# Kernel tuning notes

Hardware: AMD Instinct MI355X
Metric: run time of the kernel (lower is better)

Reference implementation:

```python
import jax, jax.numpy as jnp
import numpy as np

B, L, S = 8, 8192, 512
DQ, DC = 256, 768
H, DH = 8, 64
INNER = H * DH


def setup_inputs() -> dict:
    key = jax.random.key(0)
    ks = jax.random.split(key, 8)
    std_q = 1.0 / np.sqrt(DQ)
    std_c = 1.0 / np.sqrt(DC)
    std_o = 1.0 / np.sqrt(INNER)
    return {
        "x": jax.random.normal(ks[0], (B, L, DQ), jnp.float32),
        "context": jax.random.normal(ks[1], (B, S, DC), jnp.float32),
        "seq_lens": jax.random.randint(ks[2], (B,), 1, L + 1, jnp.int32),
        "Wq": jax.random.normal(ks[3], (DQ, INNER), jnp.float32) * std_q,
        "Wk": jax.random.normal(ks[4], (DC, INNER), jnp.float32) * std_c,
        "Wv": jax.random.normal(ks[5], (DC, INNER), jnp.float32) * std_c,
        "Wo": jax.random.normal(ks[6], (INNER, DQ), jnp.float32) * std_o,
        "bo": jnp.zeros((DQ,), jnp.float32),
    }


def reference(x, context, seq_lens, Wq, Wk, Wv, Wo, bo):
    # x: [B, L, DQ] padded jagged voxel features; seq_lens: valid count per batch.
    # Equivalent to the per-batch SDPA loop: each batch's queries attend over
    # that batch's full (unmasked) context of S tokens.
    scale = 1.0 / np.sqrt(DH)
    q = (x @ Wq).reshape(B, L, H, DH).transpose(0, 2, 1, 3)        # [B,H,L,DH]
    k = (context @ Wk).reshape(B, S, H, DH).transpose(0, 2, 1, 3)  # [B,H,S,DH]
    v = (context @ Wv).reshape(B, S, H, DH).transpose(0, 2, 1, 3)  # [B,H,S,DH]
    scores = jnp.einsum("bhld,bhsd->bhls", q, k) * scale           # [B,H,L,S]
    attn = jax.nn.softmax(scores, axis=-1)
    out = jnp.einsum("bhls,bhsd->bhld", attn, v)                   # [B,H,L,DH]
    out = out.transpose(0, 2, 1, 3).reshape(B, L, INNER)
    out = out @ Wo + bo                                            # [B,L,DQ]
    valid = (jnp.arange(L)[None, :] < seq_lens[:, None])[..., None]
    return jnp.where(valid, out, 0.0)
```

## Files before the change

kernel.cpp:

```cpp
#include <hip/hip_runtime.h>
#include <hip/hip_bf16.h>

#define DEV __device__ __forceinline__

typedef float f32x4 __attribute__((ext_vector_type(4)));
typedef unsigned short u16x4 __attribute__((ext_vector_type(4)));
typedef unsigned short u16x8 __attribute__((ext_vector_type(8)));
typedef __bf16 bf16x8 __attribute__((ext_vector_type(8)));

DEV unsigned short f2b(float f) { __bf16 h = (__bf16)f; return __builtin_bit_cast(unsigned short, h); }
DEV bf16x8 asbf8(u16x8 v) { return __builtin_bit_cast(bf16x8, v); }

#define MFMA(a, b, c) __builtin_amdgcn_mfma_f32_16x16x32_bf16((a), (b), (c), 0, 0, 0)

constexpr float QSCALE = 0.18033688011112042f;
constexpr float MFIX = 20.0f;

__global__ __launch_bounds__(256) void convert_weights(
    const float* __restrict__ Wq, const float* __restrict__ Wk,
    const float* __restrict__ Wv, const float* __restrict__ Wo,
    unsigned short* __restrict__ WqT, unsigned short* __restrict__ WkvT,
    unsigned short* __restrict__ WoT)
{
  int i = blockIdx.x * 256 + threadIdx.x;
  if (i < 131072) {
    int n = i >> 8, k = i & 255;
    WqT[i] = f2b(Wq[k * 512 + n] * QSCALE);
  } else if (i < 131072 + 786432) {
    int j = i - 131072;
    int n = j / 768, k = j - n * 768;
    float v = (n < 512) ? Wk[k * 512 + n] : Wv[k * 512 + (n - 512)];
    WkvT[j] = f2b(v);
  } else {
    int j = i - 917504;
    int n = j >> 9, k = j & 511;
    WoT[j] = f2b(Wo[k * 256 + n]);
  }
}

template<int KDIM, int NCOLS, bool AF32, int EPI>
DEV void proj_body(int bx, int by, char* smem,
                   const float* __restrict__ Af, const unsigned short* __restrict__ Ab,
                   const unsigned short* __restrict__ BT, const int* __restrict__ seq_lens,
                   unsigned short* __restrict__ out0, unsigned short* __restrict__ out1,
                   float* __restrict__ outf, const float* __restrict__ bo)
{
  constexpr int WC = NCOLS / 4;
  constexpr int NCT = WC / 16;
  constexpr int KSTEPS = KDIM / 32;
  constexpr int ASZ = AF32 ? (64 * 36 * 4) : (64 * 40 * 2);
  const int t = threadIdx.x;
  const int wid = t >> 6, lane = t & 63;
  const int q = lane & 15, g = lane >> 4;
  const int row0 = bx * 64;
  const int wcol = by * NCOLS + wid * WC;

  int sl = 0;
  if (EPI == 0 || EPI == 2) {
    sl = seq_lens[row0 >> 13];
    if ((row0 & 8191) >= sl) {
      if (EPI == 2 && by == 0) {
        f32x4 z = {0.f, 0.f, 0.f, 0.f};
        float* o = outf + (size_t)row0 * 256;
        #pragma unroll
        for (int i = 0; i < 16; ++i)
          *(f32x4*)(o + (size_t)(i * 256 + t) * 4) = z;
      }
      return;
    }
  }

  const int ar0 = t >> 3, akc = (t & 7) * 4;
  const int br0 = t >> 2, bkc = (t & 3) * 8;

  f32x4 acc[4][NCT];
  #pragma unroll
  for (int i = 0; i < 4; ++i)
    #pragma unroll
    for (int j = 0; j < NCT; ++j) acc[i][j] = {0.f, 0.f, 0.f, 0.f};

  f32x4 a0, a1;
  u16x8 ab;
  if (AF32) {
    a0 = *(const f32x4*)(Af + (size_t)(row0 + ar0) * KDIM + akc);
    a1 = *(const f32x4*)(Af + (size_t)(row0 + 32 + ar0) * KDIM + akc);
    float* Lf = (float*)smem;
    *(f32x4*)(Lf + ar0 * 36 + akc) = a0;
    *(f32x4*)(Lf + (32 + ar0) * 36 + akc) = a1;
  } else {
    ab = *(const u16x8*)(Ab + (size_t)(row0 + br0) * KDIM + bkc);
    *(u16x8*)((unsigned short*)smem + br0 * 40 + bkc) = ab;
  }
  bf16x8 bcur[NCT];
  #pragma unroll
  for (int ct = 0; ct < NCT; ++ct)
    bcur[ct] = asbf8(*(const u16x8*)(BT + (size_t)(wcol + ct * 16 + q) * KDIM + g * 8));
  __syncthreads();

  #pragma unroll 2
  for (int st = 0; st < KSTEPS; ++st) {
    const int cur = st & 1;
    const int k1 = (st + 1) * 32;

    if (st + 1 < KSTEPS) {
      if (AF32) {
        a0 = *(const f32x4*)(Af + (size_t)(row0 + ar0) * KDIM + k1 + akc);
        a1 = *(const f32x4*)(Af + (size_t)(row0 + 32 + ar0) * KDIM + k1 + akc);
      } else {
        ab = *(const u16x8*)(Ab + (size_t)(row0 + br0) * KDIM + k1 + bkc);
      }
    }
    bf16x8 bnx[NCT];
    if (st + 1 < KSTEPS) {
      #pragma unroll
      for (int ct = 0; ct < NCT; ++ct)
        bnx[ct] = asbf8(*(const u16x8*)(BT + (size_t)(wcol + ct * 16 + q) * KDIM + k1 + g * 8));
    }

    bf16x8 af[4];
    if (AF32) {
      const float* Lf = (const float*)(smem + cur * ASZ);
      #pragma unroll
      for (int rt = 0; rt < 4; ++rt) {
        const float* pp = Lf + (rt * 16 + q) * 36 + g * 8;
        f32x4 lo = *(const f32x4*)pp;
        f32x4 hi = *(const f32x4*)(pp + 4);
        u16x8 u;
        u[0] = f2b(lo[0]); u[1] = f2b(lo[1]); u[2] = f2b(lo[2]); u[3] = f2b(lo[3]);
        u[4] = f2b(hi[0]); u[5] = f2b(hi[1]); u[6] = f2b(hi[2]); u[7] = f2b(hi[3]);
        af[rt] = asbf8(u);
      }
    } else {
      const unsigned short* Lb = (const unsigned short*)(smem + cur * ASZ);
      #pragma unroll
      for (int rt = 0; rt < 4; ++rt)
        af[rt] = asbf8(*(const u16x8*)(Lb + (rt * 16 + q) * 40 + g * 8));
    }

    #pragma unroll
    for (int ct = 0; ct < NCT; ++ct)
      #pragma unroll
      for (int rt = 0; rt < 4; ++rt)
        acc[rt][ct] = MFMA(af[rt], bcur[ct], acc[rt][ct]);

    if (st + 1 < KSTEPS) {
      if (AF32) {
        float* Lf = (float*)(smem + (cur ^ 1) * ASZ);
        *(f32x4*)(Lf + ar0 * 36 + akc) = a0;
        *(f32x4*)(Lf + (32 + ar0) * 36 + akc) = a1;
      } else {
        *(u16x8*)((unsigned short*)(smem + (cur ^ 1) * ASZ) + br0 * 40 + bkc) = ab;
      }
      #pragma unroll
      for (int ct = 0; ct < NCT; ++ct) bcur[ct] = bnx[ct];
    }
    __syncthreads();
  }

  if (EPI == 0) {
    const int bb = row0 >> 13, l0 = row0 & 8191;
    #pragma unroll
    for (int ct = 0; ct < NCT; ++ct) {
      int col = wcol + ct * 16 + q;
      int hh = col >> 6, d = col & 63;
      unsigned short* o = out0 + (((size_t)bb * 8 + hh) * 8192) * 64 + d;
      #pragma unroll
      for (int rt = 0; rt < 4; ++rt)
        #pragma unroll
        for (int r = 0; r < 4; ++r) {
          int ll = l0 + rt * 16 + g * 4 + r;
          o[(size_t)ll * 64] = f2b(acc[rt][ct][r]);
        }
    }
  } else if (EPI == 1) {
    const int bb = row0 >> 9, s0 = row0 & 511;
    #pragma unroll
    for (int ct = 0; ct < NCT; ++ct) {
      int col = wcol + ct * 16 + q;
      if (col < 512) {
        int hh = col >> 6, d = col & 63;
        #pragma unroll
        for (int rt = 0; rt < 4; ++rt)
          #pragma unroll
          for (int r = 0; r < 4; ++r) {
            int s = s0 + rt * 16 + g * 4 + r;
            out0[(((size_t)bb * 8 + hh) * 512 + s) * 64 + d] = f2b(acc[rt][ct][r]);
          }
      } else {
        int c2 = col - 512, hh = c2 >> 6, d = c2 & 63;
        #pragma unroll
        for (int rt = 0; rt < 4; ++rt)
          #pragma unroll
          for (int r = 0; r < 4; ++r) {
            int s = s0 + rt * 16 + g * 4 + r;
            out1[(((size_t)bb * 8 + hh) * 64 + d) * 512 + s] = f2b(acc[rt][ct][r]);
          }
      }
    }
  } else {
    const int l0 = row0 & 8191;
    #pragma unroll
    for (int ct = 0; ct < NCT; ++ct) {
      int col = wcol + ct * 16 + q;
      float bias = bo[col];
      #pragma unroll
      for (int rt = 0; rt < 4; ++rt)
        #pragma unroll
        for (int r = 0; r < 4; ++r) {
          int ll = l0 + rt * 16 + g * 4 + r;
          float v = acc[rt][ct][r] + bias;
          outf[(size_t)(row0 + rt * 16 + g * 4 + r) * 256 + col] = (ll < sl) ? v : 0.f;
        }
    }
  }
}

__global__ __launch_bounds__(256, 3) void qkv_proj(
    const float* __restrict__ x, const float* __restrict__ ctx,
    const unsigned short* __restrict__ WqT, const unsigned short* __restrict__ WkvT,
    const int* __restrict__ seq_lens,
    unsigned short* __restrict__ Qws, unsigned short* __restrict__ Kws,
    unsigned short* __restrict__ VTws)
{
  __shared__ __align__(16) char smem[2 * (64 * 36 * 4)];
  const int bid = blockIdx.x;
  if (bid < 512) {
    proj_body<768, 128, true, 1>(bid & 63, bid >> 6, smem,
                                 ctx, nullptr, WkvT, seq_lens,
                                 Kws, VTws, nullptr, nullptr);
  } else {
    const int j = bid - 512;
    proj_body<256, 256, true, 0>(j >> 1, j & 1, smem,
                                 x, nullptr, WqT, seq_lens,
                                 Qws, nullptr, nullptr, nullptr);
  }
}

__global__ __launch_bounds__(256, 4) void o_proj(
    const unsigned short* __restrict__ AO, const unsigned short* __restrict__ WoT,
    const int* __restrict__ seq_lens, float* __restrict__ Y,
    const float* __restrict__ bo)
{
  __shared__ __align__(16) char smem[2 * (64 * 40 * 2)];
  proj_body<512, 128, false, 2>(blockIdx.x, blockIdx.y, smem,
                                nullptr, AO, WoT, seq_lens,
                                nullptr, nullptr, Y, bo);
}

__global__ __launch_bounds__(256, 4) void attn_kernel(
    const unsigned short* __restrict__ Qw, const unsigned short* __restrict__ Kw,
    const unsigned short* __restrict__ VTw, const int* __restrict__ seq_lens,
    unsigned short* __restrict__ AO)
{
  const int bid = blockIdx.x;
  const int h = bid & 7;
  const int tile = (bid >> 3) & 63;
  const int b = bid >> 9;

  const int sl = seq_lens[b];
  const int qbase0 = tile * 128;
  if (qbase0 >= sl) return;

  const int wid = threadIdx.x >> 6, lane = threadIdx.x & 63;
  const int q = lane & 15, g = lane >> 4;

  __shared__ __align__(16) unsigned short Ks[2][32 * 64];
  __shared__ __align__(16) unsigned short Vs[2][64 * 32];

  const int krow  = (wid << 3) + (lane >> 3);
  const int kslot = (lane & 7) ^ (lane >> 3);
  const int vd    = (wid << 4) + (lane >> 2);
  const int vc    = lane & 3;
  const int vswz  = (vd >> 1) & 3;
  const int vs0   = (((2 * vc) & 3) ^ vswz) * 8 + ((vc >> 1) * 4);
  const int vs1   = (((2 * vc + 1) & 3) ^ vswz) * 8 + ((vc >> 1) * 4);
  const int vrslot = (g ^ ((q >> 1) & 3)) * 8;

  const int qbase = qbase0 + wid * 32;
  const bool wactive = qbase < sl;

  const unsigned short* Qb = Qw + (((size_t)b * 8 + h) * 8192 + qbase) * 64;
  const unsigned short* Kb = Kw + ((size_t)b * 8 + h) * (512 * 64);
  const unsigned short* Vb = VTw + ((size_t)b * 8 + h) * (64 * 512);

  bf16x8 qf[2][2];
  if (wactive) {
    #pragma unroll
    for (int qt = 0; qt < 2; ++qt)
      #pragma unroll
      for (int dc = 0; dc < 2; ++dc)
        qf[qt][dc] = asbf8(*(const u16x8*)(Qb + (qt * 16 + q) * 64 + dc * 32 + g * 8));
  }

  f32x4 acc[2][4];
  float lsum[2] = {0.f, 0.f};
  #pragma unroll
  for (int qt = 0; qt < 2; ++qt)
    #pragma unroll
    for (int dt = 0; dt < 4; ++dt) acc[qt][dt] = {0.f, 0.f, 0.f, 0.f};

  {
    u16x8 kr = *(const u16x8*)(Kb + krow * 64 + (lane & 7) * 8);
    u16x8 vr = *(const u16x8*)(Vb + vd * 512 + vc * 8);
    *(u16x8*)(&Ks[0][krow * 64 + kslot * 8]) = kr;
    u16x4 vlo, vhi;
    vlo[0] = vr[0]; vlo[1] = vr[1]; vlo[2] = vr[2]; vlo[3] = vr[3];
    vhi[0] = vr[4]; vhi[1] = vr[5]; vhi[2] = vr[6]; vhi[3] = vr[7];
    *(u16x4*)(&Vs[0][vd * 32 + vs0]) = vlo;
    *(u16x4*)(&Vs[0][vd * 32 + vs1]) = vhi;
  }
  __syncthreads();

  #pragma unroll 2
  for (int st = 0; st < 16; ++st) {
    const int cur = st & 1;
    const int scn = (st + 1) * 32;

    u16x8 kn, vn;
    if (st < 15) {
      kn = *(const u16x8*)(Kb + (scn + krow) * 64 + (lane & 7) * 8);
      vn = *(const u16x8*)(Vb + vd * 512 + scn + vc * 8);
    }

    if (wactive) {
      bf16x8 kf[2][2];
      #pragma unroll
      for (int tt = 0; tt < 2; ++tt)
        #pragma unroll
        for (int dc = 0; dc < 2; ++dc)
          kf[tt][dc] = asbf8(*(const u16x8*)(
              &Ks[cur][(tt * 16 + q) * 64 + ((dc * 4 + g) ^ (q & 7)) * 8]));

      bf16x8 va[4];
      #pragma unroll
      for (int dt = 0; dt < 4; ++dt)
        va[dt] = asbf8(*(const u16x8*)(&Vs[cur][(dt * 16 + q) * 32 + vrslot]));

      #pragma unroll
      for (int qt = 0; qt < 2; ++qt) {
        f32x4 t0 = {-MFIX, -MFIX, -MFIX, -MFIX};
        f32x4 t1 = {-MFIX, -MFIX, -MFIX, -MFIX};
        t0 = MFMA(kf[0][0], qf[qt][0], t0);
        t0 = MFMA(kf[0][1], qf[qt][1], t0);
        t1 = MFMA(kf[1][0], qf[qt][0], t1);
        t1 = MFMA(kf[1][1], qf[qt][1], t1);

        float p0 = __builtin_amdgcn_exp2f(t0[0]);
        float p1 = __builtin_amdgcn_exp2f(t0[1]);
        float p2 = __builtin_amdgcn_exp2f(t0[2]);
        float p3 = __builtin_amdgcn_exp2f(t0[3]);
        float p4 = __builtin_amdgcn_exp2f(t1[0]);
        float p5 = __builtin_amdgcn_exp2f(t1[1]);
        float p6 = __builtin_amdgcn_exp2f(t1[2]);
        float p7 = __builtin_amdgcn_exp2f(t1[3]);
        lsum[qt] += ((p0 + p1) + (p2 + p3)) + ((p4 + p5) + (p6 + p7));

        u16x8 pu;
        pu[0] = f2b(p0); pu[1] = f2b(p1); pu[2] = f2b(p2); pu[3] = f2b(p3);
        pu[4] = f2b(p4); pu[5] = f2b(p5); pu[6] = f2b(p6); pu[7] = f2b(p7);
        bf16x8 pb = asbf8(pu);

        #pragma unroll
        for (int dt = 0; dt < 4; ++dt)
          acc[qt][dt] = MFMA(va[dt], pb, acc[qt][dt]);
      }
    }

    if (st < 15) {
      const int nb = cur ^ 1;
      *(u16x8*)(&Ks[nb][krow * 64 + kslot * 8]) = kn;
      u16x4 vlo, vhi;
      vlo[0] = vn[0]; vlo[1] = vn[1]; vlo[2] = vn[2]; vlo[3] = vn[3];
      vhi[0] = vn[4]; vhi[1] = vn[5]; vhi[2] = vn[6]; vhi[3] = vn[7];
      *(u16x4*)(&Vs[nb][vd * 32 + vs0]) = vlo;
      *(u16x4*)(&Vs[nb][vd * 32 + vs1]) = vhi;
    }
    __syncthreads();
  }

  if (wactive) {
    #pragma unroll
    for (int qt = 0; qt < 2; ++qt) {
      float lt = lsum[qt];
      lt += __shfl_xor(lt, 16);
      lt += __shfl_xor(lt, 32);
      float inv = __builtin_amdgcn_rcpf(lt);
      size_t ro = ((size_t)b * 8192 + qbase + qt * 16 + q) * 512 + h * 64;
      #pragma unroll
      for (int dt = 0; dt < 4; ++dt) {
        u16x4 o;
        o[0] = f2b(acc[qt][dt][0] * inv);
        o[1] = f2b(acc[qt][dt][1] * inv);
        o[2] = f2b(acc[qt][dt][2] * inv);
        o[3] = f2b(acc[qt][dt][3] * inv);
        *(u16x4*)(AO + ro + dt * 16 + g * 4) = o;
      }
    }
  }
}

extern "C" void kernel_launch(void* const* d_in, const int* in_sizes, int n_in,
                              void* d_out, int out_size, void* d_ws, size_t ws_size,
                              hipStream_t stream) {
  const float* x   = (const float*)d_in[0];
  const float* ctx = (const float*)d_in[1];
  const int*   seq = (const int*)d_in[2];
  const float* Wq  = (const float*)d_in[3];
  const float* Wk  = (const float*)d_in[4];
  const float* Wv  = (const float*)d_in[5];
  const float* Wo  = (const float*)d_in[6];
  const float* bo  = (const float*)d_in[7];
  float* Y = (float*)d_out;

  unsigned short* ws = (unsigned short*)d_ws;
  unsigned short* WqT  = ws;
  unsigned short* WkvT = WqT + 131072;
  unsigned short* WoT  = WkvT + 786432;
  unsigned short* Qws  = WoT + 131072;
  unsigned short* Kws  = Qws + 33554432;
  unsigned short* VTws = Kws + 2097152;
  unsigned short* AOws = VTws + 2097152;

  convert_weights<<<4096, 256, 0, stream>>>(Wq, Wk, Wv, Wo, WqT, WkvT, WoT);

  qkv_proj<<<2560, 256, 0, stream>>>(x, ctx, WqT, WkvT, seq, Qws, Kws, VTws);

  attn_kernel<<<4096, 256, 0, stream>>>(Qws, Kws, VTws, seq, AOws);

  o_proj<<<dim3(1024, 2), 256, 0, stream>>>(AOws, WoT, seq, Y, bo);
}
```

Baseline: 147.8 us.

## Pre-convert x and context to bf16 in a fused conversion kernel

Extends the weight conversion kernel to also convert the x and context activations to bf16 in workspace buffers, skipping x rows beyond each batch's valid length. The projection kernels then read bf16 A operands directly, which removes the in-loop fp32-to-bf16 conversion and halves A-tile shared memory. The Q projection is retiled to 128-column blocks (4608 blocks total) with higher occupancy bounds. The cost is an extra full pass that writes and rereads the converted activations through global memory.

```diff
diff --git a/kernel.cpp b/kernel.cpp
--- a/kernel.cpp
+++ b/kernel.cpp
@@ -16,39 +16,64 @@
 constexpr float QSCALE = 0.18033688011112042f;
 constexpr float MFIX = 20.0f;
 
-__global__ __launch_bounds__(256) void convert_weights(
+__global__ __launch_bounds__(256) void convert_all(
     const float* __restrict__ Wq, const float* __restrict__ Wk,
     const float* __restrict__ Wv, const float* __restrict__ Wo,
+    const float* __restrict__ x, const float* __restrict__ ctx,
+    const int* __restrict__ seq_lens,
     unsigned short* __restrict__ WqT, unsigned short* __restrict__ WkvT,
-    unsigned short* __restrict__ WoT)
+    unsigned short* __restrict__ WoT,
+    unsigned short* __restrict__ xb, unsigned short* __restrict__ ctxb)
 {
   int i = blockIdx.x * 256 + threadIdx.x;
   if (i < 131072) {
     int n = i >> 8, k = i & 255;
     WqT[i] = f2b(Wq[k * 512 + n] * QSCALE);
-  } else if (i < 131072 + 786432) {
+  } else if (i < 917504) {
     int j = i - 131072;
     int n = j / 768, k = j - n * 768;
     float v = (n < 512) ? Wk[k * 512 + n] : Wv[k * 512 + (n - 512)];
     WkvT[j] = f2b(v);
-  } else {
+  } else if (i < 1048576) {
     int j = i - 917504;
     int n = j >> 9, k = j & 511;
     WoT[j] = f2b(Wo[k * 256 + n]);
-  }
-}
-
-template<int KDIM, int NCOLS, bool AF32, int EPI>
-DEV void proj_body(int bx, int by, char* smem,
-                   const float* __restrict__ Af, const unsigned short* __restrict__ Ab,
-                   const unsigned short* __restrict__ BT, const int* __restrict__ seq_lens,
-                   unsigned short* __restrict__ out0, unsigned short* __restrict__ out1,
+  } else if (i < 1048576 + 2097152) {
+    int j = i - 1048576;
+    int base = j * 8;
+    int row = base >> 8;
+    if ((row & 8191) >= seq_lens[row >> 13]) return;
+    f32x4 lo = *(const f32x4*)(x + base);
+    f32x4 hi = *(const f32x4*)(x + base + 4);
+    u16x8 u;
+    u[0] = f2b(lo[0]); u[1] = f2b(lo[1]); u[2] = f2b(lo[2]); u[3] = f2b(lo[3]);
+    u[4] = f2b(hi[0]); u[5] = f2b(hi[1]); u[6] = f2b(hi[2]); u[7] = f2b(hi[3]);
+    *(u16x8*)(xb + base) = u;
+  } else {
+    int j = i - (1048576 + 2097152);
+    int base = j * 8;
+    f32x4 lo = *(const f32x4*)(ctx + base);
+    f32x4 hi = *(const f32x4*)(ctx + base + 4);
+    u16x8 u;
+    u[0] = f2b(lo[0]); u[1] = f2b(lo[1]); u[2] = f2b(lo[2]); u[3] = f2b(lo[3]);
+    u[4] = f2b(hi[0]); u[5] = f2b(hi[1]); u[6] = f2b(hi[2]); u[7] = f2b(hi[3]);
+    *(u16x8*)(ctxb + base) = u;
+  }
+}
+
+template<int KDIM, int NCOLS, int EPI>
+DEV void proj_bf16(int bx, int by, char* smem,
+                   const unsigned short* __restrict__ Ab,
+                   const unsigned short* __restrict__ BT,
+                   const int* __restrict__ seq_lens,
+                   unsigned short* __restrict__ out0,
+                   unsigned short* __restrict__ out1,
                    float* __restrict__ outf, const float* __restrict__ bo)
 {
   constexpr int WC = NCOLS / 4;
   constexpr int NCT = WC / 16;
   constexpr int KSTEPS = KDIM / 32;
-  constexpr int ASZ = AF32 ? (64 * 36 * 4) : (64 * 40 * 2);
+  constexpr int ASZ = 64 * 40 * 2;
   const int t = threadIdx.x;
   const int wid = t >> 6, lane = t & 63;
   const int q = lane & 15, g = lane >> 4;
@@ -70,7 +95,6 @@
     }
   }
 
-  const int ar0 = t >> 3, akc = (t & 7) * 4;
   const int br0 = t >> 2, bkc = (t & 3) * 8;
 
   f32x4 acc[4][NCT];
@@ -79,18 +103,9 @@
     #pragma unroll
     for (int j = 0; j < NCT; ++j) acc[i][j] = {0.f, 0.f, 0.f, 0.f};
 
-  f32x4 a0, a1;
   u16x8 ab;
-  if (AF32) {
-    a0 = *(const f32x4*)(Af + (size_t)(row0 + ar0) * KDIM + akc);
-    a1 = *(const f32x4*)(Af + (size_t)(row0 + 32 + ar0) * KDIM + akc);
-    float* Lf = (float*)smem;
-    *(f32x4*)(Lf + ar0 * 36 + akc) = a0;
-    *(f32x4*)(Lf + (32 + ar0) * 36 + akc) = a1;
-  } else {
-    ab = *(const u16x8*)(Ab + (size_t)(row0 + br0) * KDIM + bkc);
-    *(u16x8*)((unsigned short*)smem + br0 * 40 + bkc) = ab;
-  }
+  ab = *(const u16x8*)(Ab + (size_t)(row0 + br0) * KDIM + bkc);
+  *(u16x8*)((unsigned short*)smem + br0 * 40 + bkc) = ab;
   bf16x8 bcur[NCT];
   #pragma unroll
   for (int ct = 0; ct < NCT; ++ct)
@@ -102,14 +117,8 @@
     const int cur = st & 1;
     const int k1 = (st + 1) * 32;
 
-    if (st + 1 < KSTEPS) {
-      if (AF32) {
-        a0 = *(const f32x4*)(Af + (size_t)(row0 + ar0) * KDIM + k1 + akc);
-        a1 = *(const f32x4*)(Af + (size_t)(row0 + 32 + ar0) * KDIM + k1 + akc);
-      } else {
-        ab = *(const u16x8*)(Ab + (size_t)(row0 + br0) * KDIM + k1 + bkc);
-      }
-    }
+    if (st + 1 < KSTEPS)
+      ab = *(const u16x8*)(Ab + (size_t)(row0 + br0) * KDIM + k1 + bkc);
     bf16x8 bnx[NCT];
     if (st + 1 < KSTEPS) {
       #pragma unroll
@@ -118,19 +127,7 @@
     }
 
     bf16x8 af[4];
-    if (AF32) {
-      const float* Lf = (const float*)(smem + cur * ASZ);
-      #pragma unroll
-      for (int rt = 0; rt < 4; ++rt) {
-        const float* pp = Lf + (rt * 16 + q) * 36 + g * 8;
-        f32x4 lo = *(const f32x4*)pp;
-        f32x4 hi = *(const f32x4*)(pp + 4);
-        u16x8 u;
-        u[0] = f2b(lo[0]); u[1] = f2b(lo[1]); u[2] = f2b(lo[2]); u[3] = f2b(lo[3]);
-        u[4] = f2b(hi[0]); u[5] = f2b(hi[1]); u[6] = f2b(hi[2]); u[7] = f2b(hi[3]);
-        af[rt] = asbf8(u);
-      }
-    } else {
+    {
       const unsigned short* Lb = (const unsigned short*)(smem + cur * ASZ);
       #pragma unroll
       for (int rt = 0; rt < 4; ++rt)
@@ -144,13 +141,7 @@
         acc[rt][ct] = MFMA(af[rt], bcur[ct], acc[rt][ct]);
 
     if (st + 1 < KSTEPS) {
-      if (AF32) {
-        float* Lf = (float*)(smem + (cur ^ 1) * ASZ);
-        *(f32x4*)(Lf + ar0 * 36 + akc) = a0;
-        *(f32x4*)(Lf + (32 + ar0) * 36 + akc) = a1;
-      } else {
-        *(u16x8*)((unsigned short*)(smem + (cur ^ 1) * ASZ) + br0 * 40 + bkc) = ab;
-      }
+      *(u16x8*)((unsigned short*)(smem + (cur ^ 1) * ASZ) + br0 * 40 + bkc) = ab;
       #pragma unroll
       for (int ct = 0; ct < NCT; ++ct) bcur[ct] = bnx[ct];
     }
@@ -215,24 +206,22 @@
   }
 }
 
-__global__ __launch_bounds__(256, 3) void qkv_proj(
-    const float* __restrict__ x, const float* __restrict__ ctx,
+__global__ __launch_bounds__(256, 4) void qkv_proj(
+    const unsigned short* __restrict__ xb, const unsigned short* __restrict__ ctxb,
     const unsigned short* __restrict__ WqT, const unsigned short* __restrict__ WkvT,
     const int* __restrict__ seq_lens,
     unsigned short* __restrict__ Qws, unsigned short* __restrict__ Kws,
     unsigned short* __restrict__ VTws)
 {
-  __shared__ __align__(16) char smem[2 * (64 * 36 * 4)];
+  __shared__ __align__(16) char smem[2 * (64 * 40 * 2)];
   const int bid = blockIdx.x;
   if (bid < 512) {
-    proj_body<768, 128, true, 1>(bid & 63, bid >> 6, smem,
-                                 ctx, nullptr, WkvT, seq_lens,
-                                 Kws, VTws, nullptr, nullptr);
+    proj_bf16<768, 128, 1>(bid & 63, bid >> 6, smem,
+                           ctxb, WkvT, seq_lens, Kws, VTws, nullptr, nullptr);
   } else {
     const int j = bid - 512;
-    proj_body<256, 256, true, 0>(j >> 1, j & 1, smem,
-                                 x, nullptr, WqT, seq_lens,
-                                 Qws, nullptr, nullptr, nullptr);
+    proj_bf16<256, 128, 0>(j >> 2, j & 3, smem,
+                           xb, WqT, seq_lens, Qws, nullptr, nullptr, nullptr);
   }
 }
 
@@ -242,9 +231,8 @@
     const float* __restrict__ bo)
 {
   __shared__ __align__(16) char smem[2 * (64 * 40 * 2)];
-  proj_body<512, 128, false, 2>(blockIdx.x, blockIdx.y, smem,
-                                nullptr, AO, WoT, seq_lens,
-                                nullptr, nullptr, Y, bo);
+  proj_bf16<512, 128, 2>(blockIdx.x, blockIdx.y, smem,
+                         AO, WoT, seq_lens, nullptr, nullptr, Y, bo);
 }
 
 __global__ __launch_bounds__(256, 4) void attn_kernel(
@@ -420,10 +408,13 @@
   unsigned short* Kws  = Qws + 33554432;
   unsigned short* VTws = Kws + 2097152;
   unsigned short* AOws = VTws + 2097152;
-
-  convert_weights<<<4096, 256, 0, stream>>>(Wq, Wk, Wv, Wo, WqT, WkvT, WoT);
-
-  qkv_proj<<<2560, 256, 0, stream>>>(x, ctx, WqT, WkvT, seq, Qws, Kws, VTws);
+  unsigned short* xb   = AOws + 33554432;
+  unsigned short* ctxb = xb + 16777216;
+
+  convert_all<<<13824, 256, 0, stream>>>(Wq, Wk, Wv, Wo, x, ctx, seq,
+                                         WqT, WkvT, WoT, xb, ctxb);
+
+  qkv_proj<<<4608, 256, 0, stream>>>(xb, ctxb, WqT, WkvT, seq, Qws, Kws, VTws);
 
   attn_kernel<<<4096, 256, 0, stream>>>(Qws, Kws, VTws, seq, AOws);
 
```

Measured after the change: 152.4 us. 1.03x slower.
